# Kernel optimization log

Hardware: AMD Instinct MI355X
Metric: run time of the kernel (lower is better)

Reference implementation:

```python
import jax, jax.numpy as jnp
import numpy as np

C = 64
B, H, W = 2, 128, 512
SCALE = C ** (-0.5)


def conv1x1(x, w, b):
    # x: [B,C,H,W], w: [O,I], b: [O]
    return jnp.einsum('bihw,oi->bohw', x, w) + b[None, :, None, None]


def dwconv3x3(x, w, b):
    # depthwise 3x3, w: [C,1,3,3]
    y = jax.lax.conv_general_dilated(
        x, w, window_strides=(1, 1), padding='SAME',
        feature_group_count=x.shape[1],
        dimension_numbers=('NCHW', 'OIHW', 'NCHW'))
    return y + b[None, :, None, None]


def proj12(x, w1, b1, wd, bd):
    return dwconv3x3(conv1x1(x, w1, b1), wd, bd)


def setup_inputs() -> dict:
    key = jax.random.key(0)
    ks = jax.random.split(key, 32)
    d = {}
    d['x_l'] = jax.random.normal(ks[0], (B, C, H, W), dtype=jnp.float32)
    d['x_r'] = jax.random.normal(ks[1], (B, C, H, W), dtype=jnp.float32)
    i = 2
    for p in ['lp1', 'rp1', 'lp2', 'rp2']:
        d[p + '_w1'] = jax.random.normal(ks[i], (C, C), dtype=jnp.float32) * 0.05; i += 1
        d[p + '_b1'] = jnp.zeros((C,), dtype=jnp.float32)
        d[p + '_wd'] = jax.random.normal(ks[i], (C, 1, 3, 3), dtype=jnp.float32) * 0.1; i += 1
        d[p + '_bd'] = jnp.zeros((C,), dtype=jnp.float32)
    for p in ['lp3', 'rp3']:
        d[p + '_w'] = jax.random.normal(ks[i], (C, C), dtype=jnp.float32) * 0.05; i += 1
        d[p + '_b'] = jnp.zeros((C,), dtype=jnp.float32)
    return d


def reference(x_l, x_r,
              lp1_w1, lp1_b1, lp1_wd, lp1_bd,
              rp1_w1, rp1_b1, rp1_wd, rp1_bd,
              lp2_w1, lp2_b1, lp2_wd, lp2_bd,
              rp2_w1, rp2_b1, rp2_wd, rp2_bd,
              lp3_w, lp3_b, rp3_w, rp3_b):
    Ql = proj12(x_l, lp1_w1, lp1_b1, lp1_wd, lp1_bd)  # [B,C,H,W]
    Qr = proj12(x_r, rp1_w1, rp1_b1, rp1_wd, rp1_bd)  # [B,C,H,W]
    # attention[b,h,w,v] = sum_c Ql[b,c,h,w] * Qr[b,c,h,v]
    att = jnp.einsum('bchw,bchv->bhwv', Ql, Qr) * SCALE  # [B,H,W,W]
    Vl = proj12(x_l, lp2_w1, lp2_b1, lp2_wd, lp2_bd)
    Vr = proj12(x_r, rp2_w1, rp2_b1, rp2_wd, rp2_bd)
    # softmax over right-view width (last axis), aggregate Vr
    A_r2l = jax.nn.softmax(att, axis=-1)
    F_r2l = jnp.einsum('bhwv,bchv->bchw', A_r2l, Vr)  # [B,C,H,W]
    # transposed attention, softmax over left-view width (axis -2 of att)
    A_l2r = jax.nn.softmax(att, axis=-2)
    F_l2r = jnp.einsum('bhwv,bchw->bchv', A_l2r, Vl)  # [B,C,H,W]
    F_r2l = conv1x1(F_r2l, lp3_w, lp3_b)
    F_l2r = conv1x1(F_l2r, rp3_w, rp3_b)
    return x_l + F_r2l + x_r + F_l2r
```

## Files before the change

kernel.cpp:

```cpp
#include <hip/hip_runtime.h>
#include <hip/hip_bf16.h>

typedef __attribute__((ext_vector_type(8))) short short8;
typedef __attribute__((ext_vector_type(4))) float f32x4;

#define QSCALE 0.18033688011112042f

__device__ __forceinline__ unsigned short f2bf(float f){
    unsigned u = __float_as_uint(f);
    unsigned r = (u + 0x7fffu + ((u>>16)&1u))>>16;
    return (unsigned short)r;
}
__device__ __forceinline__ unsigned pk_rtne(float hi, float lo){
    return (((unsigned)f2bf(hi))<<16) | (unsigned)f2bf(lo);
}

__global__ __launch_bounds__(256) void init_out_k(const float* __restrict__ xl,
                                                  const float* __restrict__ xr,
                                                  float* __restrict__ out, int n4){
    int i = blockIdx.x*256 + threadIdx.x;
    if (i < n4){
        const float4* a = (const float4*)xl;
        const float4* b = (const float4*)xr;
        float4 va = a[i], vb = b[i];
        float4 vo; vo.x=va.x+vb.x; vo.y=va.y+vb.y; vo.z=va.z+vb.z; vo.w=va.w+vb.w;
        ((float4*)out)[i] = vo;
    }
}

__global__ __launch_bounds__(256) void gemm_k(const float* __restrict__ x,
                                              const float* __restrict__ wA,
                                              const float* __restrict__ bA,
                                              const float* __restrict__ wB,
                                              const float* __restrict__ bB,
                                              unsigned short* __restrict__ T1,
                                              unsigned short* __restrict__ T2){
    __shared__ __align__(16) short sA[256*72];
    __shared__ __align__(16) short sB[128*72];
    __shared__ float sbias[128];
    int tid = threadIdx.x;
    int b = blockIdx.x >> 8;
    int hw0 = (blockIdx.x & 255) << 8;
    {
        int c = tid & 63, pq = tid >> 6;
        const float* xb = x + ((size_t)b<<22) + (size_t)c*65536 + hw0;
        #pragma unroll
        for (int it=0; it<16; it++){
            int piece = pq*16 + it;
            float4 v = *(const float4*)(xb + piece*4);
            int p = piece*4;
            sA[(p+0)*72 + c] = (short)f2bf(v.x);
            sA[(p+1)*72 + c] = (short)f2bf(v.y);
            sA[(p+2)*72 + c] = (short)f2bf(v.z);
            sA[(p+3)*72 + c] = (short)f2bf(v.w);
        }
        #pragma unroll
        for (int it=0; it<32; it++){
            int lin = it*256 + tid;
            int o = lin >> 6, cc = lin & 63;
            float wv = (o < 64) ? wA[o*64 + cc] : wB[(o-64)*64 + cc];
            sB[o*72 + cc] = (short)f2bf(wv);
        }
        if (tid < 128) sbias[tid] = (tid < 64) ? bA[tid] : bB[tid-64];
    }
    __syncthreads();
    int wv = tid>>6, lane = tid&63, quad = lane>>4, l16 = lane&15;
    int m0 = wv*64;
    short8 a0[4], a1[4];
    #pragma unroll
    for (int mt=0; mt<4; mt++){
        a0[mt] = *(const short8*)(sA + (m0 + mt*16 + l16)*72 + quad*8);
        a1[mt] = *(const short8*)(sA + (m0 + mt*16 + l16)*72 + 32 + quad*8);
    }
    const f32x4 z4 = {0.f,0.f,0.f,0.f};
    int px0 = blockIdx.x << 8;
    #pragma unroll
    for (int set=0; set<2; set++){
        unsigned short* T = set ? T2 : T1;
        short8 bB0[4], bB1[4];
        #pragma unroll
        for (int nt=0; nt<4; nt++){
            bB0[nt] = *(const short8*)(sB + (set*64 + nt*16 + l16)*72 + quad*8);
            bB1[nt] = *(const short8*)(sB + (set*64 + nt*16 + l16)*72 + 32 + quad*8);
        }
        f32x4 acc[4][4];
        #pragma unroll
        for (int mt=0; mt<4; mt++)
            #pragma unroll
            for (int nt=0; nt<4; nt++){
                acc[mt][nt] = __builtin_amdgcn_mfma_f32_16x16x32_bf16(a0[mt], bB0[nt], z4, 0,0,0);
                acc[mt][nt] = __builtin_amdgcn_mfma_f32_16x16x32_bf16(a1[mt], bB1[nt], acc[mt][nt], 0,0,0);
            }
        #pragma unroll
        for (int nt=0; nt<4; nt++){
            float bias = sbias[set*64 + nt*16 + l16];
            #pragma unroll
            for (int mt=0; mt<4; mt++){
                #pragma unroll
                for (int r=0;r<4;r++){
                    int pxr = px0 + m0 + mt*16 + quad*4 + r;
                    T[(size_t)pxr*64 + nt*16 + l16] = f2bf(acc[mt][nt][r] + bias);
                }
            }
        }
    }
}

__device__ __forceinline__ void dw_tile(const unsigned short* __restrict__ Tb,
                                        const float* __restrict__ wd,
                                        const float* __restrict__ bd,
                                        int c0, int w0, int h, float acc[4][4]){
    #pragma unroll
    for (int ch=0; ch<4; ch++){
        float bv = bd[c0+ch];
        #pragma unroll
        for (int i=0;i<4;i++) acc[ch][i] = bv;
    }
    #pragma unroll
    for (int dh=-1; dh<=1; dh++){
        int hh = h + dh;
        if (hh < 0 || hh > 127) continue;
        const unsigned short* Tr = Tb + ((size_t)(hh*512))*64 + c0;
        float win[6][4];
        #pragma unroll
        for (int j=0;j<6;j++){
            int ww = w0 - 1 + j;
            if (ww >= 0 && ww < 512){
                uint2 v = *(const uint2*)(Tr + (size_t)ww*64);
                win[j][0] = __uint_as_float(v.x<<16);
                win[j][1] = __uint_as_float(v.x & 0xffff0000u);
                win[j][2] = __uint_as_float(v.y<<16);
                win[j][3] = __uint_as_float(v.y & 0xffff0000u);
            } else {
                win[j][0]=0.f; win[j][1]=0.f; win[j][2]=0.f; win[j][3]=0.f;
            }
        }
        #pragma unroll
        for (int ch=0; ch<4; ch++){
            float k0 = wd[(c0+ch)*9 + (dh+1)*3];
            float k1 = wd[(c0+ch)*9 + (dh+1)*3 + 1];
            float k2 = wd[(c0+ch)*9 + (dh+1)*3 + 2];
            #pragma unroll
            for (int i=0;i<4;i++)
                acc[ch][i] += k0*win[i][ch] + k1*win[i+1][ch] + k2*win[i+2][ch];
        }
    }
}

__global__ __launch_bounds__(256) void dwconv_k(const unsigned short* __restrict__ T1,
                                                const unsigned short* __restrict__ T2,
                                                const float* __restrict__ wd1,
                                                const float* __restrict__ bd1,
                                                const float* __restrict__ wd2,
                                                const float* __restrict__ bd2,
                                                unsigned short* __restrict__ Qdst,
                                                unsigned short* __restrict__ Vdst,
                                                float qscale){
    int bid = blockIdx.x;
    int wt = bid & 7, h = (bid>>3)&127, b = bid>>10;
    int tid = threadIdx.x;
    int cg = tid & 15, wl = tid >> 4;
    int c0 = cg*4;
    int w0 = wt*64 + wl*4;
    float acc[4][4];
    dw_tile(T1 + ((size_t)b<<22), wd1, bd1, c0, w0, h, acc);
    {
        int base = (b*128 + h)*512;
        #pragma unroll
        for (int i=0;i<4;i++){
            uint2 v;
            v.x = pk_rtne(acc[1][i]*qscale, acc[0][i]*qscale);
            v.y = pk_rtne(acc[3][i]*qscale, acc[2][i]*qscale);
            *(uint2*)(Qdst + ((size_t)(base + w0 + i))*64 + c0) = v;
        }
    }
    dw_tile(T2 + ((size_t)b<<22), wd2, bd2, c0, w0, h, acc);
    {
        #pragma unroll
        for (int ch=0; ch<4; ch++){
            uint2 v;
            v.x = pk_rtne(acc[ch][1], acc[ch][0]);
            v.y = pk_rtne(acc[ch][3], acc[ch][2]);
            *(uint2*)(Vdst + (((size_t)(b*64 + c0 + ch))<<16) + h*512 + w0) = v;
        }
    }
}

#define PQ 72
#define PK 72
#define PV 72
#define PP 72
#define PFA 72
#define POT 17
#define OFF_Q   0
#define OFF_K   18432
#define OFF_V   27648
#define LDS_TOT 36864

__global__ __launch_bounds__(256,4) void flash_k(
    const unsigned short* __restrict__ Ql, const unsigned short* __restrict__ Qr,
    const unsigned short* __restrict__ Vl, const unsigned short* __restrict__ Vr,
    const float* __restrict__ lw3, const float* __restrict__ lb3,
    const float* __restrict__ rw3, const float* __restrict__ rb3,
    float* __restrict__ out)
{
    __shared__ __align__(16) char smem[LDS_TOT];
    short* sQ  = (short*)(smem + OFF_Q);
    short* sK  = (short*)(smem + OFF_K);
    short* sV  = (short*)(smem + OFF_V);
    short* sP  = (short*)(smem + OFF_Q);
    short* sFA = (short*)(smem + OFF_Q);
    float* sOT = (float*)(smem + OFF_K);

    int bid = blockIdx.x;
    int g  = ((bid >> 5) << 3) | (bid & 7);
    int qt = (bid >> 3) & 3;
    int h = g & 127, b = (g >> 7) & 1, dir = g >> 8;
    const unsigned short *Qg, *Kg, *Vg; const float *w3, *b3;
    if (dir==0){ Qg = Ql; Kg = Qr; Vg = Vr; w3 = lw3; b3 = lb3; }
    else       { Qg = Qr; Kg = Ql; Vg = Vl; w3 = rw3; b3 = rb3; }

    int tid = threadIdx.x;
    int wv = tid>>6, lane = tid&63, quad = lane>>4, l16 = lane&15;
    int bh = b*128 + h;

    {
        const uint4* src = (const uint4*)(Qg + ((size_t)bh*512 + qt*128)*64);
        #pragma unroll
        for (int it=0; it<4; it++){
            int idx = it*256 + tid;
            int row = idx>>3, piece = idx&7;
            *(uint4*)(sQ + row*PQ + piece*8) = src[idx];
        }
    }
    __syncthreads();

    short8 aq0[2], aq1[2];
    #pragma unroll
    for (int s=0; s<2; s++){
        aq0[s] = *(const short8*)(sQ + (wv*32 + s*16 + l16)*PQ + quad*8);
        aq1[s] = *(const short8*)(sQ + (wv*32 + s*16 + l16)*PQ + 32 + quad*8);
    }

    const f32x4 z4 = {0.f,0.f,0.f,0.f};
    f32x4 oacc[2][4];
    #pragma unroll
    for (int s=0; s<2; s++)
        #pragma unroll
        for (int ct=0; ct<4; ct++) oacc[s][ct] = z4;
    float lps[2] = {0.f, 0.f};

    const uint4* Ksrc = (const uint4*)(Kg + (size_t)bh*512*64);
    const unsigned short* Vbase = Vg + ((size_t)(b*64)*128 + h)*512;

    uint4 kreg[2], vreg[2];
    #pragma unroll
    for (int it=0; it<2; it++){
        int idx = it*256 + tid;
        int row = idx>>3, piece = idx&7;
        kreg[it] = Ksrc[(size_t)row*8 + piece];
        vreg[it] = *(const uint4*)(Vbase + (size_t)row*65536 + piece*8);
    }

    for (int kt=0; kt<8; kt++){
        #pragma unroll
        for (int it=0; it<2; it++){
            int idx = it*256 + tid;
            int row = idx>>3, piece = idx&7;
            *(uint4*)(sK + row*PK + piece*8) = kreg[it];
            *(uint4*)(sV + row*PV + piece*8) = vreg[it];
        }
        __syncthreads();
        if (kt < 7){
            #pragma unroll
            for (int it=0; it<2; it++){
                int idx = it*256 + tid;
                int row = idx>>3, piece = idx&7;
                kreg[it] = Ksrc[(size_t)((kt+1)*64 + row)*8 + piece];
                vreg[it] = *(const uint4*)(Vbase + (size_t)row*65536 + (kt+1)*64 + piece*8);
            }
        }
        #pragma unroll
        for (int nt=0; nt<4; nt++){
            short8 bk0 = *(const short8*)(sK + (nt*16 + l16)*PK + quad*8);
            short8 bk1 = *(const short8*)(sK + (nt*16 + l16)*PK + 32 + quad*8);
            #pragma unroll
            for (int s=0; s<2; s++){
                f32x4 sv = __builtin_amdgcn_mfma_f32_16x16x32_bf16(bk0, aq0[s], z4, 0,0,0);
                sv       = __builtin_amdgcn_mfma_f32_16x16x32_bf16(bk1, aq1[s], sv, 0,0,0);
                float p0 = __builtin_amdgcn_exp2f(sv[0]);
                float p1 = __builtin_amdgcn_exp2f(sv[1]);
                float p2 = __builtin_amdgcn_exp2f(sv[2]);
                float p3 = __builtin_amdgcn_exp2f(sv[3]);
                lps[s] += (p0+p1) + (p2+p3);
                unsigned lo = __builtin_amdgcn_perm(__float_as_uint(p1), __float_as_uint(p0), 0x07060302);
                unsigned hi = __builtin_amdgcn_perm(__float_as_uint(p3), __float_as_uint(p2), 0x07060302);
                uint2 pv; pv.x = lo; pv.y = hi;
                *(uint2*)(sP + (wv*32 + s*16 + l16)*PP + nt*16 + quad*4) = pv;
            }
        }
        short8 ap0[2], ap1[2];
        #pragma unroll
        for (int s=0; s<2; s++){
            ap0[s] = *(const short8*)(sP + (wv*32 + s*16 + l16)*PP + quad*8);
            ap1[s] = *(const short8*)(sP + (wv*32 + s*16 + l16)*PP + 32 + quad*8);
        }
        #pragma unroll
        for (int ct=0; ct<4; ct++){
            short8 bv0 = *(const short8*)(sV + (ct*16 + l16)*PV + quad*8);
            short8 bv1 = *(const short8*)(sV + (ct*16 + l16)*PV + 32 + quad*8);
            #pragma unroll
            for (int s=0; s<2; s++){
                oacc[s][ct] = __builtin_amdgcn_mfma_f32_16x16x32_bf16(ap0[s], bv0, oacc[s][ct], 0,0,0);
                oacc[s][ct] = __builtin_amdgcn_mfma_f32_16x16x32_bf16(ap1[s], bv1, oacc[s][ct], 0,0,0);
            }
        }
        __syncthreads();
    }

    float inv[2][4];
    #pragma unroll
    for (int s=0; s<2; s++){
        float l = lps[s];
        l += __shfl_xor(l, 16);
        l += __shfl_xor(l, 32);
        #pragma unroll
        for (int r=0;r<4;r++) inv[s][r] = 1.0f / __shfl(l, quad*4 + r);
    }

    #pragma unroll
    for (int s=0; s<2; s++){
        short* sFw = sFA + (wv*32 + s*16)*PFA;
        #pragma unroll
        for (int ct=0; ct<4; ct++){
            #pragma unroll
            for (int r=0;r<4;r++)
                sFw[(quad*4+r)*PFA + ct*16 + l16] = (short)f2bf(oacc[s][ct][r]*inv[s][r]);
        }
    }
    short8 af0[2], af1[2];
    #pragma unroll
    for (int s=0; s<2; s++){
        af0[s] = *(const short8*)(sFA + (wv*32 + s*16 + l16)*PFA + quad*8);
        af1[s] = *(const short8*)(sFA + (wv*32 + s*16 + l16)*PFA + 32 + quad*8);
    }
    f32x4 d2[2][4];
    #pragma unroll
    for (int ot=0; ot<4; ot++){
        const float* wrow = w3 + (ot*16 + l16)*64 + quad*8;
        float4 wa = *(const float4*)(wrow);
        float4 wb = *(const float4*)(wrow + 4);
        float4 wc = *(const float4*)(wrow + 32);
        float4 wd = *(const float4*)(wrow + 36);
        short8 bw0, bw1;
        bw0[0]=(short)f2bf(wa.x); bw0[1]=(short)f2bf(wa.y); bw0[2]=(short)f2bf(wa.z); bw0[3]=(short)f2bf(wa.w);
        bw0[4]=(short)f2bf(wb.x); bw0[5]=(short)f2bf(wb.y); bw0[6]=(short)f2bf(wb.z); bw0[7]=(short)f2bf(wb.w);
        bw1[0]=(short)f2bf(wc.x); bw1[1]=(short)f2bf(wc.y); bw1[2]=(short)f2bf(wc.z); bw1[3]=(short)f2bf(wc.w);
        bw1[4]=(short)f2bf(wd.x); bw1[5]=(short)f2bf(wd.y); bw1[6]=(short)f2bf(wd.z); bw1[7]=(short)f2bf(wd.w);
        float bias = b3[ot*16 + l16];
        #pragma unroll
        for (int s=0; s<2; s++){
            d2[s][ot] = __builtin_amdgcn_mfma_f32_16x16x32_bf16(af0[s], bw0, z4, 0,0,0);
            d2[s][ot] = __builtin_amdgcn_mfma_f32_16x16x32_bf16(af1[s], bw1, d2[s][ot], 0,0,0);
            #pragma unroll
            for (int r=0;r<4;r++) d2[s][ot][r] += bias;
        }
    }
    float* sOw = sOT + wv*(64*POT);
    #pragma unroll
    for (int s=0; s<2; s++){
        #pragma unroll
        for (int ot=0; ot<4; ot++){
            #pragma unroll
            for (int r=0;r<4;r++)
                sOw[(ot*16 + l16)*POT + quad*4 + r] = d2[s][ot][r];
        }
        int qbase = qt*128 + wv*32 + s*16;
        #pragma unroll
        for (int it=0; it<16; it++){
            int o = it*4 + quad;
            float val = sOw[o*POT + l16];
            unsafeAtomicAdd(out + ((size_t)(b*64 + o)*128 + h)*512 + qbase + l16, val);
        }
    }
}

extern "C" void kernel_launch(void* const* d_in, const int* in_sizes, int n_in,
                              void* d_out, int out_size, void* d_ws, size_t ws_size,
                              hipStream_t stream)
{
    const float* xl = (const float*)d_in[0];
    const float* xr = (const float*)d_in[1];
    const float* lp1_w1 = (const float*)d_in[2];
    const float* lp1_b1 = (const float*)d_in[3];
    const float* lp1_wd = (const float*)d_in[4];
    const float* lp1_bd = (const float*)d_in[5];
    const float* rp1_w1 = (const float*)d_in[6];
    const float* rp1_b1 = (const float*)d_in[7];
    const float* rp1_wd = (const float*)d_in[8];
    const float* rp1_bd = (const float*)d_in[9];
    const float* lp2_w1 = (const float*)d_in[10];
    const float* lp2_b1 = (const float*)d_in[11];
    const float* lp2_wd = (const float*)d_in[12];
    const float* lp2_bd = (const float*)d_in[13];
    const float* rp2_w1 = (const float*)d_in[14];
    const float* rp2_b1 = (const float*)d_in[15];
    const float* rp2_wd = (const float*)d_in[16];
    const float* rp2_bd = (const float*)d_in[17];
    const float* lp3_w  = (const float*)d_in[18];
    const float* lp3_b  = (const float*)d_in[19];
    const float* rp3_w  = (const float*)d_in[20];
    const float* rp3_b  = (const float*)d_in[21];
    float* out = (float*)d_out;

    const size_t S = 16777216;
    char* ws = (char*)d_ws;
    unsigned short* T1  = (unsigned short*)(ws);
    unsigned short* T2  = (unsigned short*)(ws + 1*S);
    unsigned short* Ql  = (unsigned short*)(ws + 2*S);
    unsigned short* Qr  = (unsigned short*)(ws + 3*S);
    unsigned short* Vl  = (unsigned short*)(ws + 4*S);
    unsigned short* Vr  = (unsigned short*)(ws + 5*S);

    init_out_k<<<8192, 256, 0, stream>>>(xl, xr, out, 2097152);

    gemm_k<<<512, 256, 0, stream>>>(xl, lp1_w1, lp1_b1, lp2_w1, lp2_b1, T1, T2);
    dwconv_k<<<2048, 256, 0, stream>>>(T1, T2, lp1_wd, lp1_bd, lp2_wd, lp2_bd, Ql, Vl, QSCALE);

    gemm_k<<<512, 256, 0, stream>>>(xr, rp1_w1, rp1_b1, rp2_w1, rp2_b1, T1, T2);
    dwconv_k<<<2048, 256, 0, stream>>>(T1, T2, rp1_wd, rp1_bd, rp2_wd, rp2_bd, Qr, Vr, 1.0f);

    flash_k<<<2048, 256, 0, stream>>>(Ql, Qr, Vl, Vr, lp3_w, lp3_b, rp3_w, rp3_b, out);
}
```

Measured before the change: 363.8 us.

## Fuse input transpose into residual init, merge both-side GEMMs, drop flash prefetch

A new prep kernel writes the x_l+x_r residual and also transposes both inputs to pixel-major bf16. A single gemm launch then covers both views and loads those tiles with contiguous 16-byte copies instead of strided fp32 converts. Workspace buffers are reused across stages, cutting one kernel launch. In flash_k the register double-buffer prefetch of K/V is removed and the 4-wave occupancy hint is dropped, which lowers register pressure but exposes global load latency before each tile.

```diff
diff --git a/kernel.cpp b/kernel.cpp
--- a/kernel.cpp
+++ b/kernel.cpp
@@ -15,44 +15,97 @@
     return (((unsigned)f2bf(hi))<<16) | (unsigned)f2bf(lo);
 }
 
-__global__ __launch_bounds__(256) void init_out_k(const float* __restrict__ xl,
-                                                  const float* __restrict__ xr,
-                                                  float* __restrict__ out, int n4){
-    int i = blockIdx.x*256 + threadIdx.x;
-    if (i < n4){
-        const float4* a = (const float4*)xl;
-        const float4* b = (const float4*)xr;
-        float4 va = a[i], vb = b[i];
+__global__ __launch_bounds__(256) void prep_k(const float* __restrict__ xl,
+                                              const float* __restrict__ xr,
+                                              float* __restrict__ out,
+                                              unsigned short* __restrict__ XtL,
+                                              unsigned short* __restrict__ XtR){
+    __shared__ float ft[64*65];
+    int bid = blockIdx.x;
+    int strip = bid & 1023, b = bid >> 10;
+    int px0 = strip << 6;
+    int tid = threadIdx.x;
+    float4 vrs[4];
+    #pragma unroll
+    for (int it=0; it<4; it++){
+        int lin = it*256 + tid;
+        int c = lin >> 4, piece = lin & 15;
+        size_t off = (((size_t)(b*64 + c))<<16) + px0 + piece*4;
+        float4 va = *(const float4*)(xl + off);
+        float4 vb = *(const float4*)(xr + off);
+        vrs[it] = vb;
         float4 vo; vo.x=va.x+vb.x; vo.y=va.y+vb.y; vo.z=va.z+vb.z; vo.w=va.w+vb.w;
-        ((float4*)out)[i] = vo;
-    }
-}
-
-__global__ __launch_bounds__(256) void gemm_k(const float* __restrict__ x,
-                                              const float* __restrict__ wA,
-                                              const float* __restrict__ bA,
-                                              const float* __restrict__ wB,
-                                              const float* __restrict__ bB,
-                                              unsigned short* __restrict__ T1,
-                                              unsigned short* __restrict__ T2){
+        *(float4*)(out + off) = vo;
+        float* d = ft + c*65 + piece*4;
+        d[0]=va.x; d[1]=va.y; d[2]=va.z; d[3]=va.w;
+    }
+    __syncthreads();
+    #pragma unroll
+    for (int it=0; it<2; it++){
+        int lin = it*256 + tid;
+        int pxl = lin >> 3, cb = lin & 7;
+        unsigned r[4];
+        #pragma unroll
+        for (int j=0;j<4;j++){
+            unsigned lo = f2bf(ft[(cb*8 + 2*j  )*65 + pxl]);
+            unsigned hi = f2bf(ft[(cb*8 + 2*j+1)*65 + pxl]);
+            r[j] = lo | (hi<<16);
+        }
+        uint4 v; v.x=r[0]; v.y=r[1]; v.z=r[2]; v.w=r[3];
+        *(uint4*)(XtL + ((size_t)(b<<16) + px0 + pxl)*64 + cb*8) = v;
+    }
+    __syncthreads();
+    #pragma unroll
+    for (int it=0; it<4; it++){
+        int lin = it*256 + tid;
+        int c = lin >> 4, piece = lin & 15;
+        float4 vb = vrs[it];
+        float* d = ft + c*65 + piece*4;
+        d[0]=vb.x; d[1]=vb.y; d[2]=vb.z; d[3]=vb.w;
+    }
+    __syncthreads();
+    #pragma unroll
+    for (int it=0; it<2; it++){
+        int lin = it*256 + tid;
+        int pxl = lin >> 3, cb = lin & 7;
+        unsigned r[4];
+        #pragma unroll
+        for (int j=0;j<4;j++){
+            unsigned lo = f2bf(ft[(cb*8 + 2*j  )*65 + pxl]);
+            unsigned hi = f2bf(ft[(cb*8 + 2*j+1)*65 + pxl]);
+            r[j] = lo | (hi<<16);
+        }
+        uint4 v; v.x=r[0]; v.y=r[1]; v.z=r[2]; v.w=r[3];
+        *(uint4*)(XtR + ((size_t)(b<<16) + px0 + pxl)*64 + cb*8) = v;
+    }
+}
+
+__global__ __launch_bounds__(256) void gemm_k(const unsigned short* __restrict__ XtL,
+                                              const unsigned short* __restrict__ XtR,
+                                              const float* __restrict__ wAL, const float* __restrict__ bAL,
+                                              const float* __restrict__ wBL, const float* __restrict__ bBL,
+                                              const float* __restrict__ wAR, const float* __restrict__ bAR,
+                                              const float* __restrict__ wBR, const float* __restrict__ bBR,
+                                              unsigned short* __restrict__ T1L, unsigned short* __restrict__ T2L,
+                                              unsigned short* __restrict__ T1R, unsigned short* __restrict__ T2R){
     __shared__ __align__(16) short sA[256*72];
     __shared__ __align__(16) short sB[128*72];
     __shared__ float sbias[128];
     int tid = threadIdx.x;
-    int b = blockIdx.x >> 8;
-    int hw0 = (blockIdx.x & 255) << 8;
+    int side = blockIdx.x >> 9;
+    int px0 = (blockIdx.x & 511) << 8;
+    const unsigned short* Xt = side ? XtR : XtL;
+    const float* wA = side ? wAR : wAL;  const float* bA = side ? bAR : bAL;
+    const float* wB = side ? wBR : wBL;  const float* bB = side ? bBR : bBL;
+    unsigned short* T1 = side ? T1R : T1L;
+    unsigned short* T2 = side ? T2R : T2L;
     {
-        int c = tid & 63, pq = tid >> 6;
-        const float* xb = x + ((size_t)b<<22) + (size_t)c*65536 + hw0;
-        #pragma unroll
-        for (int it=0; it<16; it++){
-            int piece = pq*16 + it;
-            float4 v = *(const float4*)(xb + piece*4);
-            int p = piece*4;
-            sA[(p+0)*72 + c] = (short)f2bf(v.x);
-            sA[(p+1)*72 + c] = (short)f2bf(v.y);
-            sA[(p+2)*72 + c] = (short)f2bf(v.z);
-            sA[(p+3)*72 + c] = (short)f2bf(v.w);
+        const uint4* src = (const uint4*)(Xt + (size_t)px0*64);
+        #pragma unroll
+        for (int it=0; it<8; it++){
+            int lin = it*256 + tid;
+            int row = lin >> 3, piece = lin & 7;
+            *(uint4*)(sA + row*72 + piece*8) = src[lin];
         }
         #pragma unroll
         for (int it=0; it<32; it++){
@@ -73,7 +126,6 @@
         a1[mt] = *(const short8*)(sA + (m0 + mt*16 + l16)*72 + 32 + quad*8);
     }
     const f32x4 z4 = {0.f,0.f,0.f,0.f};
-    int px0 = blockIdx.x << 8;
     #pragma unroll
     for (int set=0; set<2; set++){
         unsigned short* T = set ? T2 : T1;
@@ -197,7 +249,7 @@
 #define OFF_V   27648
 #define LDS_TOT 36864
 
-__global__ __launch_bounds__(256,4) void flash_k(
+__global__ __launch_bounds__(256) void flash_k(
     const unsigned short* __restrict__ Ql, const unsigned short* __restrict__ Qr,
     const unsigned short* __restrict__ Vl, const unsigned short* __restrict__ Vr,
     const float* __restrict__ lw3, const float* __restrict__ lb3,
@@ -253,33 +305,16 @@
     const uint4* Ksrc = (const uint4*)(Kg + (size_t)bh*512*64);
     const unsigned short* Vbase = Vg + ((size_t)(b*64)*128 + h)*512;
 
-    uint4 kreg[2], vreg[2];
-    #pragma unroll
-    for (int it=0; it<2; it++){
-        int idx = it*256 + tid;
-        int row = idx>>3, piece = idx&7;
-        kreg[it] = Ksrc[(size_t)row*8 + piece];
-        vreg[it] = *(const uint4*)(Vbase + (size_t)row*65536 + piece*8);
-    }
-
     for (int kt=0; kt<8; kt++){
         #pragma unroll
         for (int it=0; it<2; it++){
             int idx = it*256 + tid;
             int row = idx>>3, piece = idx&7;
-            *(uint4*)(sK + row*PK + piece*8) = kreg[it];
-            *(uint4*)(sV + row*PV + piece*8) = vreg[it];
+            *(uint4*)(sK + row*PK + piece*8) = Ksrc[(size_t)(kt*64 + row)*8 + piece];
+            uint4 vv = *(const uint4*)(Vbase + (size_t)row*65536 + kt*64 + piece*8);
+            *(uint4*)(sV + row*PV + piece*8) = vv;
         }
         __syncthreads();
-        if (kt < 7){
-            #pragma unroll
-            for (int it=0; it<2; it++){
-                int idx = it*256 + tid;
-                int row = idx>>3, piece = idx&7;
-                kreg[it] = Ksrc[(size_t)((kt+1)*64 + row)*8 + piece];
-                vreg[it] = *(const uint4*)(Vbase + (size_t)row*65536 + (kt+1)*64 + piece*8);
-            }
-        }
         #pragma unroll
         for (int nt=0; nt<4; nt++){
             short8 bk0 = *(const short8*)(sK + (nt*16 + l16)*PK + quad*8);
@@ -415,20 +450,26 @@
 
     const size_t S = 16777216;
     char* ws = (char*)d_ws;
-    unsigned short* T1  = (unsigned short*)(ws);
-    unsigned short* T2  = (unsigned short*)(ws + 1*S);
-    unsigned short* Ql  = (unsigned short*)(ws + 2*S);
-    unsigned short* Qr  = (unsigned short*)(ws + 3*S);
-    unsigned short* Vl  = (unsigned short*)(ws + 4*S);
-    unsigned short* Vr  = (unsigned short*)(ws + 5*S);
-
-    init_out_k<<<8192, 256, 0, stream>>>(xl, xr, out, 2097152);
-
-    gemm_k<<<512, 256, 0, stream>>>(xl, lp1_w1, lp1_b1, lp2_w1, lp2_b1, T1, T2);
-    dwconv_k<<<2048, 256, 0, stream>>>(T1, T2, lp1_wd, lp1_bd, lp2_wd, lp2_bd, Ql, Vl, QSCALE);
-
-    gemm_k<<<512, 256, 0, stream>>>(xr, rp1_w1, rp1_b1, rp2_w1, rp2_b1, T1, T2);
-    dwconv_k<<<2048, 256, 0, stream>>>(T1, T2, rp1_wd, rp1_bd, rp2_wd, rp2_bd, Qr, Vr, 1.0f);
-
-    flash_k<<<2048, 256, 0, stream>>>(Ql, Qr, Vl, Vr, lp3_w, lp3_b, rp3_w, rp3_b, out);
-}
+    unsigned short* s0 = (unsigned short*)(ws);
+    unsigned short* s1 = (unsigned short*)(ws + 1*S);
+    unsigned short* s2 = (unsigned short*)(ws + 2*S);
+    unsigned short* s3 = (unsigned short*)(ws + 3*S);
+    unsigned short* s4 = (unsigned short*)(ws + 4*S);
+    unsigned short* s5 = (unsigned short*)(ws + 5*S);
+
+    prep_k<<<2048, 256, 0, stream>>>(xl, xr, out, s0, s1);
+
+    gemm_k<<<1024, 256, 0, stream>>>(s0, s1,
+        lp1_w1, lp1_b1, lp2_w1, lp2_b1,
+        rp1_w1, rp1_b1, rp2_w1, rp2_b1,
+        s2, s3, s4, s5);
+
+    dwconv_k<<<2048, 256, 0, stream>>>(s2, s3,
+        lp1_wd, lp1_bd, lp2_wd, lp2_bd, s0, s1, QSCALE);
+
+    dwconv_k<<<2048, 256, 0, stream>>>(s4, s5,
+        rp1_wd, rp1_bd, rp2_wd, rp2_bd, s2, s3, 1.0f);
+
+    flash_k<<<2048, 256, 0, stream>>>(s0, s2, s1, s3,
+        lp3_w, lp3_b, rp3_w, rp3_b, out);
+}
```

Result: faster. 326.9 us (-10.1%).
